# Performance work log

Hardware: AMD Instinct MI355X
Metric: run time of the kernel (lower is better)

## Reference

```python
import jax, jax.numpy as jnp
import numpy as np

N_NODES = 50000
N_EDGES = 800000
NFEAT = 512
NHID = 128


def gcn_conv(x, W, b, src, dst, n_nodes):
    """PyG-style GCNConv: self-loops + symmetric deg^{-1/2} normalization."""
    # degrees over edges incl. self-loops (src/dst already contain them)
    deg = jax.ops.segment_sum(jnp.ones_like(src, dtype=x.dtype), dst,
                              num_segments=n_nodes)
    dinv = jnp.where(deg > 0, jax.lax.rsqrt(deg), 0.0)
    norm = dinv[src] * dinv[dst]            # [E+N]
    h = x @ W                               # [N, out] dense transform first (out <= in)
    msgs = h[src] * norm[:, None]           # gather + scale
    out = jax.ops.segment_sum(msgs, dst, num_segments=n_nodes)  # scatter-add
    return out + b


def setup_inputs() -> dict:
    key = jax.random.key(0)
    k1, k2, k3, k4 = jax.random.split(key, 4)
    x = jax.random.normal(k1, (N_NODES, NFEAT), dtype=jnp.float32)
    edge_index = jax.random.randint(k2, (2, N_EDGES), 0, N_NODES, dtype=jnp.int64)
    W1 = jax.random.normal(k3, (NFEAT, 2 * NHID), dtype=jnp.float32) / np.sqrt(NFEAT)
    b1 = jnp.zeros((2 * NHID,), dtype=jnp.float32)
    W2 = jax.random.normal(k4, (2 * NHID, NHID), dtype=jnp.float32) / np.sqrt(2 * NHID)
    b2 = jnp.zeros((NHID,), dtype=jnp.float32)
    return {"x": x, "edge_index": edge_index, "W1": W1, "b1": b1, "W2": W2, "b2": b2}


def reference(x, edge_index, W1, b1, W2, b2):
    n = x.shape[0]
    loop = jnp.arange(n, dtype=edge_index.dtype)
    src = jnp.concatenate([edge_index[0], loop])  # add self-loops once, reuse per layer
    dst = jnp.concatenate([edge_index[1], loop])
    h = jax.nn.relu(gcn_conv(x, W1, b1, src, dst, n))
    # dropout is identity in eval mode (reference runs in inference mode)
    out = gcn_conv(h, W2, b2, src, dst, n)
    return out
```

## Files before the change

### kernel.cpp

```cpp
#include <hip/hip_runtime.h>
#include <cstdint>
#include <cstddef>

#define NFEAT 512
#define NH1   256
#define NH2   128

#define P_CHUNKS 128
#define HHALF    25088
#define NP       (2 * HHALF)
#define HPB      1024

typedef __attribute__((ext_vector_type(8))) short short8;
typedef __attribute__((ext_vector_type(4))) float float4v;

__device__ __forceinline__ unsigned short f2bf(float f) {
    unsigned int u = __float_as_uint(f);
    u += 0x7fffu + ((u >> 16) & 1u);
    return (unsigned short)(u >> 16);
}
__device__ __forceinline__ float bf2f(unsigned short u) {
    return __uint_as_float(((unsigned int)u) << 16);
}

__device__ __forceinline__ void load_lds16(const void* g, void* l) {
    __builtin_amdgcn_global_load_lds(
        (const __attribute__((address_space(1))) void*)g,
        (__attribute__((address_space(3))) void*)l, 16, 0, 0);
}

__global__ __launch_bounds__(HPB) void k_hist_cvtw(
    const int* __restrict__ dst, int* __restrict__ hist,
    const float* __restrict__ W1, unsigned short* __restrict__ W1t,
    const float* __restrict__ W2, unsigned short* __restrict__ W2t,
    int E, int CE, int HB) {
    __shared__ int lh[HHALF];
    if (blockIdx.x >= HB) {
        const int i = (blockIdx.x - HB) * HPB + (int)threadIdx.x;
        const int T1 = NFEAT * NH1;
        const int T2 = NH1 * NH2;
        if (i < T1) {
            const int k = i / NH1, n = i % NH1;
            W1t[(size_t)n * NFEAT + k] = f2bf(W1[i]);
        } else if (i < T1 + T2) {
            const int j = i - T1;
            const int k = j / NH2, n = j % NH2;
            W2t[(size_t)n * NH1 + k] = f2bf(W2[j]);
        }
        return;
    }
    const int c    = blockIdx.x >> 1;
    const int hf   = blockIdx.x & 1;
    const int base = hf * HHALF;
    for (int i = threadIdx.x; i < HHALF; i += HPB) lh[i] = 0;
    __syncthreads();
    const int lo = c * CE;
    const int hi = lo + CE < E ? lo + CE : E;
    for (int e = lo + (int)threadIdx.x; e < hi; e += HPB) {
        const int d = dst[e] - base;
        if ((unsigned)d < (unsigned)HHALF) atomicAdd(&lh[d], 1);
    }
    __syncthreads();
    int* outp = hist + (size_t)c * NP + base;
    for (int i = threadIdx.x; i < HHALF; i += HPB) outp[i] = lh[i];
}

__global__ __launch_bounds__(256) void k_redscan1(
    const int* __restrict__ hist, int* __restrict__ degi,
    float* __restrict__ dinv, int* __restrict__ blocksums, int N) {
    __shared__ int red[256];
    const int t = threadIdx.x;
    const int d = blockIdx.x * 256 + t;
    int s = 0;
    if (d < N) {
#pragma unroll 8
        for (int c = 0; c < P_CHUNKS; ++c) s += hist[(size_t)c * NP + d];
        degi[d] = s;
        dinv[d] = rsqrtf((float)(s + 1));
    }
    red[t] = s;
    __syncthreads();
    for (int off = 128; off > 0; off >>= 1) {
        if (t < off) red[t] += red[t + off];
        __syncthreads();
    }
    if (t == 0) blocksums[blockIdx.x] = red[0];
}

__global__ __launch_bounds__(1024) void k_scan2(
    const int* __restrict__ blocksums, int* __restrict__ blockoffs,
    int* __restrict__ row_start, int nb, int N) {
    __shared__ int sm[1024];
    const int t = threadIdx.x;
    const int v = (t < nb) ? blocksums[t] : 0;
    sm[t] = v;
    __syncthreads();
    for (int off = 1; off < 1024; off <<= 1) {
        const int x = (t >= off) ? sm[t - off] : 0;
        __syncthreads();
        sm[t] += x;
        __syncthreads();
    }
    if (t < nb) blockoffs[t] = sm[t] - v;
    if (t == 1023) row_start[N] = sm[1023];
}

__global__ __launch_bounds__(256) void k_scan3off(
    const int* __restrict__ degi, const int* __restrict__ blockoffs,
    int* __restrict__ row_start, int* __restrict__ hist, int N) {
    __shared__ int tsum[256];
    const int t = threadIdx.x;
    const int d = blockIdx.x * 256 + t;
    const int v = (d < N) ? degi[d] : 0;
    tsum[t] = v;
    __syncthreads();
    for (int off = 1; off < 256; off <<= 1) {
        const int x = (t >= off) ? tsum[t - off] : 0;
        __syncthreads();
        tsum[t] += x;
        __syncthreads();
    }
    if (d < N) {
        int run = blockoffs[blockIdx.x] + tsum[t] - v;
        row_start[d] = run;
        for (int c = 0; c < P_CHUNKS; ++c) {
            int* p = &hist[(size_t)c * NP + d];
            const int tt = *p;
            *p = run;
            run += tt;
        }
    }
}

__global__ __launch_bounds__(HPB) void k_place(const int* __restrict__ src,
                                               const int* __restrict__ dst,
                                               const int* __restrict__ hist,
                                               int* __restrict__ csr_src, int E, int CE) {
    __shared__ int lcur[HHALF];
    const int c    = blockIdx.x >> 1;
    const int hf   = blockIdx.x & 1;
    const int base = hf * HHALF;
    const int* offp = hist + (size_t)c * NP + base;
    for (int i = threadIdx.x; i < HHALF; i += HPB) lcur[i] = offp[i];
    __syncthreads();
    const int lo = c * CE;
    const int hi = lo + CE < E ? lo + CE : E;
    for (int e = lo + (int)threadIdx.x; e < hi; e += HPB) {
        const int d = dst[e] - base;
        if ((unsigned)d < (unsigned)HHALF) {
            const int p = atomicAdd(&lcur[d], 1);
            csr_src[p] = src[e];
        }
    }
}

__global__ __launch_bounds__(512) void gemm_x_fused(
    const float* __restrict__ x, const float* __restrict__ dinv,
    const unsigned short* __restrict__ Bt, unsigned short* __restrict__ C,
    int Nrows, int K) {
    __shared__ unsigned short As[128 * 32];
    __shared__ unsigned short Bs[256 * 32];
    const int t    = threadIdx.x;
    const int wave = t >> 6, lane = t & 63;
    const int row0 = blockIdx.x * 128;
    const int quad = lane >> 4, l15 = lane & 15;
    const int wm = (wave >> 2) * 64;
    const int wn = (wave & 3) * 64;

    const int arow = t >> 2;
    const int ak   = (t & 3) * 8;
    const int gr   = (row0 + arow < Nrows) ? row0 + arow : Nrows - 1;
    const float wd = dinv[gr];
    const float* gx = x + (size_t)gr * K + ak;
    unsigned short* lA = &As[arow * 32 + ak];

    const int brow = t >> 2;
    const int bk   = (t & 3) * 8;
    const unsigned short* gB0 = Bt + (size_t)brow * K + bk;
    const unsigned short* gB1 = Bt + (size_t)(128 + brow) * K + bk;
    unsigned short* lB0 = &Bs[wave * 512];
    unsigned short* lB1 = &Bs[128 * 32 + wave * 512];

    float4v acc[4][4] = {};

    for (int k0 = 0; k0 < K; k0 += 32) {
        __syncthreads();
        load_lds16(gB0 + k0, lB0);
        load_lds16(gB1 + k0, lB1);
        const float4 v0 = *(const float4*)(gx + k0);
        const float4 v1 = *(const float4*)(gx + k0 + 4);
        short8 o;
        o[0] = (short)f2bf(v0.x * wd); o[1] = (short)f2bf(v0.y * wd);
        o[2] = (short)f2bf(v0.z * wd); o[3] = (short)f2bf(v0.w * wd);
        o[4] = (short)f2bf(v1.x * wd); o[5] = (short)f2bf(v1.y * wd);
        o[6] = (short)f2bf(v1.z * wd); o[7] = (short)f2bf(v1.w * wd);
        *(short8*)lA = o;
        __syncthreads();

        short8 a[4], b[4];
#pragma unroll
        for (int i = 0; i < 4; ++i) {
            a[i] = *(const short8*)&As[(wm + i * 16 + l15) * 32 + quad * 8];
            b[i] = *(const short8*)&Bs[(wn + i * 16 + l15) * 32 + quad * 8];
        }
#pragma unroll
        for (int mt = 0; mt < 4; ++mt)
#pragma unroll
            for (int nt = 0; nt < 4; ++nt)
                acc[mt][nt] = __builtin_amdgcn_mfma_f32_16x16x32_bf16(
                    a[mt], b[nt], acc[mt][nt], 0, 0, 0);
    }

#pragma unroll
    for (int mt = 0; mt < 4; ++mt) {
#pragma unroll
        for (int nt = 0; nt < 4; ++nt) {
            const int c = wn + nt * 16 + l15;
#pragma unroll
            for (int r = 0; r < 4; ++r) {
                const int row = row0 + wm + mt * 16 + quad * 4 + r;
                C[(size_t)row * NH1 + c] = f2bf(acc[mt][nt][r]);
            }
        }
    }
}

__global__ __launch_bounds__(256) void gemm_bf16(
    const unsigned short* __restrict__ A, const unsigned short* __restrict__ Bt,
    unsigned short* __restrict__ C, int N, int K) {
    __shared__ unsigned short As[128 * 32];
    __shared__ unsigned short Bs[128 * 32];
    const int t    = threadIdx.x;
    const int wave = t >> 6, lane = t & 63;
    const int row0 = blockIdx.y * 128, col0 = blockIdx.x * 128;
    const int wm = (wave >> 1) * 64, wn = (wave & 1) * 64;
    const int sr = lane >> 2;
    const int sk = (lane & 3) * 8;
    const int quad = lane >> 4, l15 = lane & 15;

    const int ca = wave * 2;
    const unsigned short* gA0 = A  + (size_t)(row0 + ca * 16 + sr) * K + sk;
    const unsigned short* gA1 = gA0 + (size_t)16 * K;
    const unsigned short* gB0 = Bt + (size_t)(col0 + ca * 16 + sr) * K + sk;
    const unsigned short* gB1 = gB0 + (size_t)16 * K;
    unsigned short* lA0 = &As[ca * 512];
    unsigned short* lA1 = &As[(ca + 1) * 512];
    unsigned short* lB0 = &Bs[ca * 512];
    unsigned short* lB1 = &Bs[(ca + 1) * 512];

    float4v acc[4][4] = {};

    for (int k0 = 0; k0 < K; k0 += 32) {
        __syncthreads();
        load_lds16(gA0 + k0, lA0);
        load_lds16(gA1 + k0, lA1);
        load_lds16(gB0 + k0, lB0);
        load_lds16(gB1 + k0, lB1);
        __syncthreads();

        short8 a[4], b[4];
#pragma unroll
        for (int i = 0; i < 4; ++i) {
            a[i] = *(const short8*)&As[(wm + i * 16 + l15) * 32 + quad * 8];
            b[i] = *(const short8*)&Bs[(wn + i * 16 + l15) * 32 + quad * 8];
        }
#pragma unroll
        for (int mt = 0; mt < 4; ++mt)
#pragma unroll
            for (int nt = 0; nt < 4; ++nt)
                acc[mt][nt] = __builtin_amdgcn_mfma_f32_16x16x32_bf16(
                    a[mt], b[nt], acc[mt][nt], 0, 0, 0);
    }

#pragma unroll
    for (int mt = 0; mt < 4; ++mt) {
#pragma unroll
        for (int nt = 0; nt < 4; ++nt) {
            const int c = col0 + wn + nt * 16 + l15;
#pragma unroll
            for (int r = 0; r < 4; ++r) {
                const int row = row0 + wm + mt * 16 + quad * 4 + r;
                C[(size_t)row * N + c] = f2bf(acc[mt][nt][r]);
            }
        }
    }
}

template <int F, bool RELU, bool OUTF32>
__global__ __launch_bounds__(256) void k_gather(
    const int* __restrict__ row_start, const int* __restrict__ csr_src,
    const float* __restrict__ dinv, const unsigned short* __restrict__ h,
    const float* __restrict__ bias, unsigned short* __restrict__ ob,
    float* __restrict__ of, int N) {
    const int gid  = blockIdx.x * blockDim.x + threadIdx.x;
    const int node = gid >> 6;
    const int lane = gid & 63;
    if (node >= N) return;

    constexpr int EL = F / 64;
    const float wd = dinv[node];
    const int jb = row_start[node];
    const int je = row_start[node + 1];
    const unsigned short* hl = h + (size_t)lane * EL;

    float acc[EL];
    {
        const unsigned short* hp = hl + (size_t)node * F;
        if (EL == 4) {
            const ushort4 v = *(const ushort4*)hp;
            acc[0] = bf2f(v.x); acc[1] = bf2f(v.y);
            acc[2] = bf2f(v.z); acc[3] = bf2f(v.w);
        } else {
            const ushort2 v = *(const ushort2*)hp;
            acc[0] = bf2f(v.x); acc[1] = bf2f(v.y);
        }
    }

    for (int j0 = jb; j0 < je; j0 += 64) {
        int jj = j0 + lane;
        if (jj >= je) jj = je - 1;
        const int myi = csr_src[jj];
        const int rem = je - j0;
        const int cnt = rem < 64 ? rem : 64;
        int i = 0;
        for (; i + 8 <= cnt; i += 8) {
            int s[8];
#pragma unroll
            for (int u = 0; u < 8; ++u) s[u] = __shfl(myi, i + u);
            if (EL == 4) {
                ushort4 v[8];
#pragma unroll
                for (int u = 0; u < 8; ++u)
                    v[u] = *(const ushort4*)(hl + (size_t)s[u] * F);
#pragma unroll
                for (int u = 0; u < 8; ++u) {
                    acc[0] += bf2f(v[u].x); acc[1] += bf2f(v[u].y);
                    acc[2] += bf2f(v[u].z); acc[3] += bf2f(v[u].w);
                }
            } else {
                ushort2 v[8];
#pragma unroll
                for (int u = 0; u < 8; ++u)
                    v[u] = *(const ushort2*)(hl + (size_t)s[u] * F);
#pragma unroll
                for (int u = 0; u < 8; ++u) {
                    acc[0] += bf2f(v[u].x); acc[1] += bf2f(v[u].y);
                }
            }
        }
        for (; i + 4 <= cnt; i += 4) {
            const int s0 = __shfl(myi, i + 0);
            const int s1 = __shfl(myi, i + 1);
            const int s2 = __shfl(myi, i + 2);
            const int s3 = __shfl(myi, i + 3);
            if (EL == 4) {
                const ushort4 v0 = *(const ushort4*)(hl + (size_t)s0 * F);
                const ushort4 v1 = *(const ushort4*)(hl + (size_t)s1 * F);
                const ushort4 v2 = *(const ushort4*)(hl + (size_t)s2 * F);
                const ushort4 v3 = *(const ushort4*)(hl + (size_t)s3 * F);
                acc[0] += bf2f(v0.x) + bf2f(v1.x) + bf2f(v2.x) + bf2f(v3.x);
                acc[1] += bf2f(v0.y) + bf2f(v1.y) + bf2f(v2.y) + bf2f(v3.y);
                acc[2] += bf2f(v0.z) + bf2f(v1.z) + bf2f(v2.z) + bf2f(v3.z);
                acc[3] += bf2f(v0.w) + bf2f(v1.w) + bf2f(v2.w) + bf2f(v3.w);
            } else {
                const ushort2 v0 = *(const ushort2*)(hl + (size_t)s0 * F);
                const ushort2 v1 = *(const ushort2*)(hl + (size_t)s1 * F);
                const ushort2 v2 = *(const ushort2*)(hl + (size_t)s2 * F);
                const ushort2 v3 = *(const ushort2*)(hl + (size_t)s3 * F);
                acc[0] += bf2f(v0.x) + bf2f(v1.x) + bf2f(v2.x) + bf2f(v3.x);
                acc[1] += bf2f(v0.y) + bf2f(v1.y) + bf2f(v2.y) + bf2f(v3.y);
            }
        }
        for (; i < cnt; ++i) {
            const int s = __shfl(myi, i);
            const unsigned short* hp = hl + (size_t)s * F;
            if (EL == 4) {
                const ushort4 v = *(const ushort4*)hp;
                acc[0] += bf2f(v.x); acc[1] += bf2f(v.y);
                acc[2] += bf2f(v.z); acc[3] += bf2f(v.w);
            } else {
                const ushort2 v = *(const ushort2*)hp;
                acc[0] += bf2f(v.x); acc[1] += bf2f(v.y);
            }
        }
    }

#pragma unroll
    for (int i = 0; i < EL; ++i) {
        float v = fmaf(acc[i], wd, bias[lane * EL + i]);
        if (OUTF32) {
            of[(size_t)node * F + lane * EL + i] = v;
        } else {
            if (RELU) v = fmaxf(v, 0.f);
            ob[(size_t)node * F + lane * EL + i] = f2bf(v * wd);
        }
    }
}

extern "C" void kernel_launch(void* const* d_in, const int* in_sizes, int n_in,
                              void* d_out, int out_size, void* d_ws, size_t ws_size,
                              hipStream_t stream) {
    const float* x   = (const float*)d_in[0];
    const int*   ei  = (const int*)d_in[1];
    const float* W1  = (const float*)d_in[2];
    const float* b1  = (const float*)d_in[3];
    const float* W2  = (const float*)d_in[4];
    const float* b2  = (const float*)d_in[5];
    float*       out = (float*)d_out;

    const int N = in_sizes[0] / NFEAT;
    const int E = in_sizes[1] / 2;
    const int Mp = ((N + 127) / 128) * 128;
    const int* srcp = ei;
    const int* dstp = ei + E;
    const int CE = (E + P_CHUNKS - 1) / P_CHUNKS;
    const int nRed = (N + 255) / 256;

    char* wsb = (char*)d_ws;
    auto take = [&](size_t bytes) {
        char* p = wsb;
        wsb += (bytes + 255) & ~(size_t)255;
        return p;
    };
    int*   degi      = (int*)take((size_t)N * 4);
    int*   row_start = (int*)take((size_t)(N + 1) * 4);
    int*   csr_src   = (int*)take((size_t)E * 4);
    int*   blocksums = (int*)take((size_t)1024 * 4);
    int*   blockoffs = (int*)take((size_t)1024 * 4);
    float* dinv      = (float*)take((size_t)N * 4);
    unsigned short* h2r = (unsigned short*)take((size_t)Mp * NH2 * 2);
    unsigned short* W1t = (unsigned short*)take((size_t)NH1 * NFEAT * 2);
    unsigned short* W2t = (unsigned short*)take((size_t)NH2 * NH1 * 2);
    const size_t hBytes    = (size_t)Mp * NH1 * 2;
    const size_t histBytes = (size_t)P_CHUNKS * NP * 4;
    char* big = take(histBytes > 2 * hBytes ? histBytes : 2 * hBytes);
    int*            hist = (int*)big;
    unsigned short* h    = (unsigned short*)big;
    unsigned short* h1   = (unsigned short*)(big + hBytes);
    unsigned short* h2   = h2r;

    for (int rep = 0; rep < 2; ++rep) {
        const int HB = P_CHUNKS * 2;
        const int CB = (NFEAT * NH1 + NH1 * NH2 + HPB - 1) / HPB;
        k_hist_cvtw<<<HB + CB, HPB, 0, stream>>>(dstp, hist, W1, W1t, W2, W2t,
                                                 E, CE, HB);
        k_redscan1<<<nRed, 256, 0, stream>>>(hist, degi, dinv, blocksums, N);
        k_scan2<<<1, 1024, 0, stream>>>(blocksums, blockoffs, row_start, nRed, N);
        k_scan3off<<<nRed, 256, 0, stream>>>(degi, blockoffs, row_start, hist, N);
        k_place<<<P_CHUNKS * 2, HPB, 0, stream>>>(srcp, dstp, hist, csr_src, E, CE);
    }

    gemm_x_fused<<<Mp / 128, 512, 0, stream>>>(x, dinv, W1t, h, N, NFEAT);
    {
        int total = N * 64;
        k_gather<NH1, true, false><<<(total + 255) / 256, 256, 0, stream>>>(
            row_start, csr_src, dinv, h, b1, h1, nullptr, N);
    }

    {
        dim3 g(NH2 / 128, Mp / 128);
        gemm_bf16<<<g, 256, 0, stream>>>(h1, W2t, h2, NH2, NH1);
    }
    {
        int total = N * 64;
        k_gather<NH2, false, true><<<(total + 255) / 256, 256, 0, stream>>>(
            row_start, csr_src, dinv, h2, b2, nullptr, out, N);
    }
}
```

Measured before the change: 360.4 us.

## Slice gather across feature blocks per half-wave and drop duplicated CSR build

```diff
diff --git a/kernel.cpp b/kernel.cpp
--- a/kernel.cpp
+++ b/kernel.cpp
@@ -286,114 +286,57 @@
     }
 }
 
-template <int F, bool RELU, bool OUTF32>
-__global__ __launch_bounds__(256) void k_gather(
+template <int F, int NSL, int LSH, bool RELU, bool OUTF32>
+__global__ __launch_bounds__(256) void k_gather_x(
     const int* __restrict__ row_start, const int* __restrict__ csr_src,
     const float* __restrict__ dinv, const unsigned short* __restrict__ h,
     const float* __restrict__ bias, unsigned short* __restrict__ ob,
     float* __restrict__ of, int N) {
-    const int gid  = blockIdx.x * blockDim.x + threadIdx.x;
-    const int node = gid >> 6;
-    const int lane = gid & 63;
+    const int slice = blockIdx.x & (NSL - 1);
+    const int ng    = blockIdx.x >> LSH;
+    const int hw    = threadIdx.x >> 5;
+    const int l31   = threadIdx.x & 31;
+    const int node  = ng * 8 + hw;
     if (node >= N) return;
-
-    constexpr int EL = F / 64;
+    const int feat  = slice * 32 + l31;
+
     const float wd = dinv[node];
     const int jb = row_start[node];
     const int je = row_start[node + 1];
-    const unsigned short* hl = h + (size_t)lane * EL;
-
-    float acc[EL];
-    {
-        const unsigned short* hp = hl + (size_t)node * F;
-        if (EL == 4) {
-            const ushort4 v = *(const ushort4*)hp;
-            acc[0] = bf2f(v.x); acc[1] = bf2f(v.y);
-            acc[2] = bf2f(v.z); acc[3] = bf2f(v.w);
-        } else {
-            const ushort2 v = *(const ushort2*)hp;
-            acc[0] = bf2f(v.x); acc[1] = bf2f(v.y);
-        }
-    }
-
-    for (int j0 = jb; j0 < je; j0 += 64) {
-        int jj = j0 + lane;
+    const unsigned short* hf = h + feat;
+
+    float acc = bf2f(hf[(size_t)node * F]);
+
+    for (int j0 = jb; j0 < je; j0 += 32) {
+        int jj = j0 + l31;
         if (jj >= je) jj = je - 1;
         const int myi = csr_src[jj];
         const int rem = je - j0;
-        const int cnt = rem < 64 ? rem : 64;
+        const int cnt = rem < 32 ? rem : 32;
         int i = 0;
-        for (; i + 8 <= cnt; i += 8) {
-            int s[8];
-#pragma unroll
-            for (int u = 0; u < 8; ++u) s[u] = __shfl(myi, i + u);
-            if (EL == 4) {
-                ushort4 v[8];
-#pragma unroll
-                for (int u = 0; u < 8; ++u)
-                    v[u] = *(const ushort4*)(hl + (size_t)s[u] * F);
-#pragma unroll
-                for (int u = 0; u < 8; ++u) {
-                    acc[0] += bf2f(v[u].x); acc[1] += bf2f(v[u].y);
-                    acc[2] += bf2f(v[u].z); acc[3] += bf2f(v[u].w);
-                }
-            } else {
-                ushort2 v[8];
-#pragma unroll
-                for (int u = 0; u < 8; ++u)
-                    v[u] = *(const ushort2*)(hl + (size_t)s[u] * F);
-#pragma unroll
-                for (int u = 0; u < 8; ++u) {
-                    acc[0] += bf2f(v[u].x); acc[1] += bf2f(v[u].y);
-                }
-            }
-        }
         for (; i + 4 <= cnt; i += 4) {
-            const int s0 = __shfl(myi, i + 0);
-            const int s1 = __shfl(myi, i + 1);
-            const int s2 = __shfl(myi, i + 2);
-            const int s3 = __shfl(myi, i + 3);
-            if (EL == 4) {
-                const ushort4 v0 = *(const ushort4*)(hl + (size_t)s0 * F);
-                const ushort4 v1 = *(const ushort4*)(hl + (size_t)s1 * F);
-                const ushort4 v2 = *(const ushort4*)(hl + (size_t)s2 * F);
-                const ushort4 v3 = *(const ushort4*)(hl + (size_t)s3 * F);
-                acc[0] += bf2f(v0.x) + bf2f(v1.x) + bf2f(v2.x) + bf2f(v3.x);
-                acc[1] += bf2f(v0.y) + bf2f(v1.y) + bf2f(v2.y) + bf2f(v3.y);
-                acc[2] += bf2f(v0.z) + bf2f(v1.z) + bf2f(v2.z) + bf2f(v3.z);
-                acc[3] += bf2f(v0.w) + bf2f(v1.w) + bf2f(v2.w) + bf2f(v3.w);
-            } else {
-                const ushort2 v0 = *(const ushort2*)(hl + (size_t)s0 * F);
-                const ushort2 v1 = *(const ushort2*)(hl + (size_t)s1 * F);
-                const ushort2 v2 = *(const ushort2*)(hl + (size_t)s2 * F);
-                const ushort2 v3 = *(const ushort2*)(hl + (size_t)s3 * F);
-                acc[0] += bf2f(v0.x) + bf2f(v1.x) + bf2f(v2.x) + bf2f(v3.x);
-                acc[1] += bf2f(v0.y) + bf2f(v1.y) + bf2f(v2.y) + bf2f(v3.y);
-            }
+            const int s0 = __shfl(myi, i + 0, 32);
+            const int s1 = __shfl(myi, i + 1, 32);
+            const int s2 = __shfl(myi, i + 2, 32);
+            const int s3 = __shfl(myi, i + 3, 32);
+            const float v0 = bf2f(hf[(size_t)s0 * F]);
+            const float v1 = bf2f(hf[(size_t)s1 * F]);
+            const float v2 = bf2f(hf[(size_t)s2 * F]);
+            const float v3 = bf2f(hf[(size_t)s3 * F]);
+            acc += v0 + v1 + v2 + v3;
         }
         for (; i < cnt; ++i) {
-            const int s = __shfl(myi, i);
-            const unsigned short* hp = hl + (size_t)s * F;
-            if (EL == 4) {
-                const ushort4 v = *(const ushort4*)hp;
-                acc[0] += bf2f(v.x); acc[1] += bf2f(v.y);
-                acc[2] += bf2f(v.z); acc[3] += bf2f(v.w);
-            } else {
-                const ushort2 v = *(const ushort2*)hp;
-                acc[0] += bf2f(v.x); acc[1] += bf2f(v.y);
-            }
-        }
-    }
-
-#pragma unroll
-    for (int i = 0; i < EL; ++i) {
-        float v = fmaf(acc[i], wd, bias[lane * EL + i]);
-        if (OUTF32) {
-            of[(size_t)node * F + lane * EL + i] = v;
-        } else {
-            if (RELU) v = fmaxf(v, 0.f);
-            ob[(size_t)node * F + lane * EL + i] = f2bf(v * wd);
-        }
+            const int s = __shfl(myi, i, 32);
+            acc += bf2f(hf[(size_t)s * F]);
+        }
+    }
+
+    float v = fmaf(acc, wd, bias[feat]);
+    if (OUTF32) {
+        of[(size_t)node * F + feat] = v;
+    } else {
+        if (RELU) v = fmaxf(v, 0.f);
+        ob[(size_t)node * F + feat] = f2bf(v * wd);
     }
 }
 
@@ -415,6 +358,7 @@
     const int* dstp = ei + E;
     const int CE = (E + P_CHUNKS - 1) / P_CHUNKS;
     const int nRed = (N + 255) / 256;
+    const int nodeGroups = (N + 7) / 8;
 
     char* wsb = (char*)d_ws;
     auto take = [&](size_t bytes) {
@@ -439,31 +383,25 @@
     unsigned short* h1   = (unsigned short*)(big + hBytes);
     unsigned short* h2   = h2r;
 
-    for (int rep = 0; rep < 2; ++rep) {
+    {
         const int HB = P_CHUNKS * 2;
         const int CB = (NFEAT * NH1 + NH1 * NH2 + HPB - 1) / HPB;
         k_hist_cvtw<<<HB + CB, HPB, 0, stream>>>(dstp, hist, W1, W1t, W2, W2t,
                                                  E, CE, HB);
-        k_redscan1<<<nRed, 256, 0, stream>>>(hist, degi, dinv, blocksums, N);
-        k_scan2<<<1, 1024, 0, stream>>>(blocksums, blockoffs, row_start, nRed, N);
-        k_scan3off<<<nRed, 256, 0, stream>>>(degi, blockoffs, row_start, hist, N);
-        k_place<<<P_CHUNKS * 2, HPB, 0, stream>>>(srcp, dstp, hist, csr_src, E, CE);
-    }
+    }
+    k_redscan1<<<nRed, 256, 0, stream>>>(hist, degi, dinv, blocksums, N);
+    k_scan2<<<1, 1024, 0, stream>>>(blocksums, blockoffs, row_start, nRed, N);
+    k_scan3off<<<nRed, 256, 0, stream>>>(degi, blockoffs, row_start, hist, N);
+    k_place<<<P_CHUNKS * 2, HPB, 0, stream>>>(srcp, dstp, hist, csr_src, E, CE);
 
     gemm_x_fused<<<Mp / 128, 512, 0, stream>>>(x, dinv, W1t, h, N, NFEAT);
-    {
-        int total = N * 64;
-        k_gather<NH1, true, false><<<(total + 255) / 256, 256, 0, stream>>>(
-            row_start, csr_src, dinv, h, b1, h1, nullptr, N);
-    }
+    k_gather_x<NH1, 8, 3, true, false><<<nodeGroups * 8, 256, 0, stream>>>(
+        row_start, csr_src, dinv, h, b1, h1, nullptr, N);
 
     {
         dim3 g(NH2 / 128, Mp / 128);
         gemm_bf16<<<g, 256, 0, stream>>>(h1, W2t, h2, NH2, NH1);
     }
-    {
-        int total = N * 64;
-        k_gather<NH2, false, true><<<(total + 255) / 256, 256, 0, stream>>>(
-            row_start, csr_src, dinv, h2, b2, nullptr, out, N);
-    }
-}
+    k_gather_x<NH2, 4, 2, false, true><<<nodeGroups * 4, 256, 0, stream>>>(
+        row_start, csr_src, dinv, h2, b2, nullptr, out, N);
+}
```

New measurement: 395.2 us. +9.6%, slower.
